# Performance work log

Hardware: AMD Instinct MI355X
Metric: run time of the kernel (lower is better)

## Reference

```python
import jax, jax.numpy as jnp
import numpy as np

N = 131072          # total atoms/nodes
LSQ = 9             # (lmax+1)^2 spherical coefficients
C = 128             # sphere_channels
H = 1024            # hidden_channels
NUM_MOLS = 2048     # number of molecules (len(natoms))


def setup_inputs() -> dict:
    key = jax.random.key(0)
    ks = jax.random.split(key, 8)
    node_embedding = jax.random.normal(ks[0], (N, LSQ, C), dtype=jnp.float32)
    batch = jnp.sort(jax.random.randint(ks[1], (N,), 0, NUM_MOLS, dtype=jnp.int64))
    natoms = jax.random.randint(ks[2], (NUM_MOLS,), 1, 100, dtype=jnp.int64)
    # MLP parameters (Linear weights stored as [in, out] for x @ W + b)
    s1 = 1.0 / np.sqrt(C)
    s2 = 1.0 / np.sqrt(H)
    W1 = jax.random.uniform(ks[3], (C, H), jnp.float32, -s1, s1)
    b1 = jnp.zeros((H,), jnp.float32)
    W2 = jax.random.uniform(ks[4], (H, H), jnp.float32, -s2, s2)
    b2 = jnp.zeros((H,), jnp.float32)
    W3 = jax.random.uniform(ks[5], (H, 1), jnp.float32, -s2, s2)
    b3 = jnp.zeros((1,), jnp.float32)
    return {"node_embedding": node_embedding, "W1": W1, "b1": b1,
            "W2": W2, "b2": b2, "W3": W3, "b3": b3,
            "batch": batch, "natoms": natoms}


def reference(node_embedding, W1, b1, W2, b2, W3, b3, batch, natoms):
    # take l=0 coefficient: [N, C]
    x = node_embedding[:, 0, :]
    h = jax.nn.silu(x @ W1 + b1)          # [N, H]
    h = jax.nn.silu(h @ W2 + b2)          # [N, H]
    node_energy = (h @ W3 + b3)[:, 0]     # [N]
    # scatter-sum per molecule (index_add_)
    energy = jax.ops.segment_sum(node_energy, batch, num_segments=NUM_MOLS)
    return energy  # reduce == 'sum'
```

## Files before the change

### kernel.cpp

```cpp
#include <hip/hip_runtime.h>

typedef unsigned short u16;
typedef __attribute__((ext_vector_type(8))) short bf16x8;
typedef __attribute__((ext_vector_type(4))) float f32x4;

#define NROWS 131072
#define NMOL  2048
#define CIN   128
#define HDIM  1024
#define BM    64
#define EMBSTRIDE 1152

__device__ __forceinline__ u16 f2bf(float f) {
    union { float f; unsigned u; } v; v.f = f;
    unsigned u = v.u;
    u += 0x7FFFu + ((u >> 16) & 1u);
    return (u16)(u >> 16);
}

__device__ __forceinline__ float silu_f(float v) {
    float e = __expf(-v);
    return v * __builtin_amdgcn_rcpf(1.0f + e);
}

__device__ __forceinline__ f32x4 mfma16(bf16x8 a, bf16x8 b, f32x4 c) {
    return __builtin_amdgcn_mfma_f32_16x16x32_bf16(a, b, c, 0, 0, 0);
}

__global__ void pack_w(const float* __restrict__ W, u16* __restrict__ dst, int K, int N) {
    int tid  = blockIdx.x * blockDim.x + threadIdx.x;
    int lane = tid & 63;
    int frag = tid >> 6;
    int KT = K >> 5;
    int NT = N >> 4;
    if (frag >= KT * NT) return;
    int kt = frag % KT;
    int nt = frag / KT;
    int col  = (nt << 4) + (lane & 15);
    int krow = (kt << 5) + ((lane >> 4) << 3);
    __align__(16) u16 tmp[8];
    #pragma unroll
    for (int j = 0; j < 8; ++j) tmp[j] = f2bf(W[(size_t)(krow + j) * N + col]);
    *reinterpret_cast<uint4*>(dst + (size_t)tid * 8) = *reinterpret_cast<uint4*>(tmp);
}

__global__ __launch_bounds__(512, 2) void fused_mlp(
    const float* __restrict__ emb,
    const u16*  __restrict__ w1f,
    const u16*  __restrict__ w2f,
    const float* __restrict__ b1,
    const float* __restrict__ b2,
    const float* __restrict__ w3,
    const float* __restrict__ b3,
    float* __restrict__ node_e)
{
    __shared__ u16  x_lds[BM][CIN + 8];
    __shared__ u16  h1_lds[BM][HDIM + 8];
    __shared__ float e_red[8][BM];

    const int tid  = threadIdx.x;
    const int lane = tid & 63;
    const int w    = tid >> 6;
    const int row0 = blockIdx.x * BM;

    {
        int r   = tid >> 3;
        int seg = tid & 7;
        const float4* s4 = reinterpret_cast<const float4*>(
            emb + (size_t)(row0 + r) * EMBSTRIDE + seg * 16);
        __align__(16) u16 u[16];
        #pragma unroll
        for (int i = 0; i < 4; ++i) {
            float4 f = s4[i];
            u[i*4+0] = f2bf(f.x); u[i*4+1] = f2bf(f.y);
            u[i*4+2] = f2bf(f.z); u[i*4+3] = f2bf(f.w);
        }
        uint4* d = reinterpret_cast<uint4*>(&x_lds[r][seg * 16]);
        d[0] = reinterpret_cast<uint4*>(u)[0];
        d[1] = reinterpret_cast<uint4*>(u)[1];
        reinterpret_cast<float*>(e_red)[tid] = 0.0f;
    }
    __syncthreads();

    {
        bf16x8 a1[4][4];
        #pragma unroll
        for (int mt = 0; mt < 4; ++mt)
            #pragma unroll
            for (int kt = 0; kt < 4; ++kt)
                a1[mt][kt] = *reinterpret_cast<const bf16x8*>(
                    &x_lds[mt*16 + (lane & 15)][kt*32 + ((lane >> 4) << 3)]);

        #pragma unroll
        for (int ntl = 0; ntl < 8; ++ntl) {
            int nt  = w * 8 + ntl;
            int col = nt * 16 + (lane & 15);
            float bias = b1[col];
            f32x4 acc[4];
            #pragma unroll
            for (int mt = 0; mt < 4; ++mt) acc[mt] = (f32x4){0.f, 0.f, 0.f, 0.f};
            #pragma unroll
            for (int kt = 0; kt < 4; ++kt) {
                bf16x8 bfrag = *reinterpret_cast<const bf16x8*>(
                    w1f + ((size_t)(nt * 4 + kt) * 64 + lane) * 8);
                #pragma unroll
                for (int mt = 0; mt < 4; ++mt)
                    acc[mt] = mfma16(a1[mt][kt], bfrag, acc[mt]);
            }
            #pragma unroll
            for (int mt = 0; mt < 4; ++mt)
                #pragma unroll
                for (int j = 0; j < 4; ++j) {
                    float s = silu_f(acc[mt][j] + bias);
                    h1_lds[mt*16 + (lane >> 4)*4 + j][col] = f2bf(s);
                }
        }
    }
    __syncthreads();

    float e_lane[16];
    #pragma unroll
    for (int i = 0; i < 16; ++i) e_lane[i] = 0.0f;

    const u16* aptr = &h1_lds[lane & 15][(lane >> 4) << 3];

    #pragma unroll
    for (int c = 0; c < 2; ++c) {
        int ntbase = w * 8 + c * 4;
        f32x4 acc[4][4];
        #pragma unroll
        for (int mt = 0; mt < 4; ++mt)
            #pragma unroll
            for (int nti = 0; nti < 4; ++nti) acc[mt][nti] = (f32x4){0.f, 0.f, 0.f, 0.f};

        #pragma unroll 2
        for (int kt = 0; kt < 32; ++kt) {
            bf16x8 a[4];
            #pragma unroll
            for (int mt = 0; mt < 4; ++mt)
                a[mt] = *reinterpret_cast<const bf16x8*>(aptr + mt*16*(HDIM+8) + kt*32);
            #pragma unroll
            for (int nti = 0; nti < 4; ++nti) {
                bf16x8 b = *reinterpret_cast<const bf16x8*>(
                    w2f + (((size_t)(ntbase + nti) * 32 + kt) * 64 + lane) * 8);
                #pragma unroll
                for (int mt = 0; mt < 4; ++mt)
                    acc[mt][nti] = mfma16(a[mt], b, acc[mt][nti]);
            }
        }
        #pragma unroll
        for (int nti = 0; nti < 4; ++nti) {
            int col = (ntbase + nti) * 16 + (lane & 15);
            float bias = b2[col];
            float w3v  = w3[col];
            #pragma unroll
            for (int mt = 0; mt < 4; ++mt)
                #pragma unroll
                for (int j = 0; j < 4; ++j) {
                    float s = silu_f(acc[mt][nti][j] + bias);
                    e_lane[mt*4 + j] += s * w3v;
                }
        }
    }

    #pragma unroll
    for (int off = 1; off < 16; off <<= 1)
        #pragma unroll
        for (int i = 0; i < 16; ++i)
            e_lane[i] += __shfl_xor(e_lane[i], off, 64);

    if ((lane & 15) == 0) {
        int g = lane >> 4;
        #pragma unroll
        for (int mt = 0; mt < 4; ++mt)
            #pragma unroll
            for (int j = 0; j < 4; ++j)
                e_red[w][mt*16 + g*4 + j] = e_lane[mt*4 + j];
    }
    __syncthreads();

    if (tid < BM) {
        float s = 0.0f;
        #pragma unroll
        for (int ww = 0; ww < 8; ++ww) s += e_red[ww][tid];
        node_e[row0 + tid] = s + b3[0];
    }
}

__global__ void segsum(const float* __restrict__ node_e,
                       const int* __restrict__ batch,
                       float* __restrict__ out)
{
    int mol  = blockIdx.x;
    int lane = threadIdx.x;

    int lo = 0, hi = NROWS;
    while (lo < hi) { int mid = (lo + hi) >> 1; if (batch[mid] < mol)     lo = mid + 1; else hi = mid; }
    int start = lo;
    lo = start; hi = NROWS;
    while (lo < hi) { int mid = (lo + hi) >> 1; if (batch[mid] < mol + 1) lo = mid + 1; else hi = mid; }
    int end = lo;

    float s = 0.0f;
    for (int i = start + lane; i < end; i += 64) s += node_e[i];
    #pragma unroll
    for (int off = 32; off; off >>= 1) s += __shfl_xor(s, off, 64);
    if (lane == 0) out[mol] = s;
}

extern "C" void kernel_launch(void* const* d_in, const int* in_sizes, int n_in,
                              void* d_out, int out_size, void* d_ws, size_t ws_size,
                              hipStream_t stream) {
    const float* emb = (const float*)d_in[0];
    const float* W1  = (const float*)d_in[1];
    const float* b1  = (const float*)d_in[2];
    const float* W2  = (const float*)d_in[3];
    const float* b2  = (const float*)d_in[4];
    const float* W3  = (const float*)d_in[5];
    const float* b3  = (const float*)d_in[6];
    const int*   batch = (const int*)d_in[7];

    u16* w1f = (u16*)d_ws;
    u16* w2f = (u16*)((char*)d_ws + (size_t)CIN * HDIM * 2);
    float* node_e = (float*)((char*)d_ws + (size_t)CIN * HDIM * 2 + (size_t)HDIM * HDIM * 2);

    pack_w<<<64,  256, 0, stream>>>(W1, w1f, CIN,  HDIM);
    pack_w<<<512, 256, 0, stream>>>(W2, w2f, HDIM, HDIM);
    fused_mlp<<<NROWS / BM, 512, 0, stream>>>(emb, w1f, w2f, b1, b2, W3, b3, node_e);
    segsum<<<NMOL, 64, 0, stream>>>(node_e, batch, (float*)d_out);
}
```

Before: 337.6 us.

## Switch fused MLP to 32x32x16 MFMA tiles with software-pipelined operand loads

Replaces the 16x16x32 bf16 MFMA tiling with 32x32x16 tiles, so each wave covers 64 rows by 128 columns in a single pass. The weight packing layout is rewritten to match. Weight and activation fragments are double-buffered, loading step k+1 or k+2 while step k computes, to hide global and LDS load latency. The larger accumulators raise register pressure, and the wider 32-lane shuffle reduction adds work in the epilogue.

```diff
diff --git a/kernel.cpp b/kernel.cpp
--- a/kernel.cpp
+++ b/kernel.cpp
@@ -1,8 +1,8 @@
 #include <hip/hip_runtime.h>
 
 typedef unsigned short u16;
-typedef __attribute__((ext_vector_type(8))) short bf16x8;
-typedef __attribute__((ext_vector_type(4))) float f32x4;
+typedef __attribute__((ext_vector_type(8)))  short bf16x8;
+typedef __attribute__((ext_vector_type(16))) float f32x16;
 
 #define NROWS 131072
 #define NMOL  2048
@@ -11,6 +11,10 @@
 #define BM    64
 #define EMBSTRIDE 1152
 
+#define KT1 (CIN  / 16)
+#define KT2 (HDIM / 16)
+#define NT  (HDIM / 32)
+
 __device__ __forceinline__ u16 f2bf(float f) {
     union { float f; unsigned u; } v; v.f = f;
     unsigned u = v.u;
@@ -23,21 +27,21 @@
     return v * __builtin_amdgcn_rcpf(1.0f + e);
 }
 
-__device__ __forceinline__ f32x4 mfma16(bf16x8 a, bf16x8 b, f32x4 c) {
-    return __builtin_amdgcn_mfma_f32_16x16x32_bf16(a, b, c, 0, 0, 0);
-}
-
-__global__ void pack_w(const float* __restrict__ W, u16* __restrict__ dst, int K, int N) {
+__device__ __forceinline__ f32x16 mfma32(bf16x8 a, bf16x8 b, f32x16 c) {
+    return __builtin_amdgcn_mfma_f32_32x32x16_bf16(a, b, c, 0, 0, 0);
+}
+
+__global__ void pack_w32(const float* __restrict__ W, u16* __restrict__ dst, int K, int N) {
     int tid  = blockIdx.x * blockDim.x + threadIdx.x;
     int lane = tid & 63;
     int frag = tid >> 6;
-    int KT = K >> 5;
-    int NT = N >> 4;
-    if (frag >= KT * NT) return;
-    int kt = frag % KT;
-    int nt = frag / KT;
-    int col  = (nt << 4) + (lane & 15);
-    int krow = (kt << 5) + ((lane >> 4) << 3);
+    int NTl = N >> 5;
+    int KTl = K >> 4;
+    if (frag >= KTl * NTl) return;
+    int kt = frag / NTl;
+    int nt = frag - kt * NTl;
+    int col  = (nt << 5) + (lane & 31);
+    int krow = (kt << 4) + ((lane >> 5) << 3);
     __align__(16) u16 tmp[8];
     #pragma unroll
     for (int j = 0; j < 8; ++j) tmp[j] = f2bf(W[(size_t)(krow + j) * N + col]);
@@ -61,6 +65,8 @@
     const int tid  = threadIdx.x;
     const int lane = tid & 63;
     const int w    = tid >> 6;
+    const int l31  = lane & 31;
+    const int lhi  = lane >> 5;
     const int row0 = blockIdx.x * BM;
 
     {
@@ -78,104 +84,156 @@
         uint4* d = reinterpret_cast<uint4*>(&x_lds[r][seg * 16]);
         d[0] = reinterpret_cast<uint4*>(u)[0];
         d[1] = reinterpret_cast<uint4*>(u)[1];
-        reinterpret_cast<float*>(e_red)[tid] = 0.0f;
-    }
+    }
+
+    auto LDB1 = [&](int kt, bf16x8* b) {
+        #pragma unroll
+        for (int nti = 0; nti < 4; ++nti)
+            b[nti] = *reinterpret_cast<const bf16x8*>(
+                w1f + (((size_t)kt * NT + w * 4 + nti) * 64 + lane) * 8);
+    };
+    auto LDB2 = [&](int kt, bf16x8* b) {
+        #pragma unroll
+        for (int nti = 0; nti < 4; ++nti)
+            b[nti] = *reinterpret_cast<const bf16x8*>(
+                w2f + (((size_t)kt * NT + w * 4 + nti) * 64 + lane) * 8);
+    };
+
+    bf16x8 bC[4], bN[4];
+    LDB1(0, bC);
     __syncthreads();
 
     {
-        bf16x8 a1[4][4];
-        #pragma unroll
-        for (int mt = 0; mt < 4; ++mt)
-            #pragma unroll
-            for (int kt = 0; kt < 4; ++kt)
-                a1[mt][kt] = *reinterpret_cast<const bf16x8*>(
-                    &x_lds[mt*16 + (lane & 15)][kt*32 + ((lane >> 4) << 3)]);
-
-        #pragma unroll
-        for (int ntl = 0; ntl < 8; ++ntl) {
-            int nt  = w * 8 + ntl;
-            int col = nt * 16 + (lane & 15);
+        f32x16 acc1[2][4];
+        #pragma unroll
+        for (int mt = 0; mt < 2; ++mt)
+            #pragma unroll
+            for (int nti = 0; nti < 4; ++nti)
+                #pragma unroll
+                for (int r = 0; r < 16; ++r) acc1[mt][nti][r] = 0.0f;
+
+        #pragma unroll
+        for (int kt = 0; kt < KT1; ++kt) {
+            if (kt + 1 < KT1) LDB1(kt + 1, bN);
+            bf16x8 a[2];
+            #pragma unroll
+            for (int mt = 0; mt < 2; ++mt)
+                a[mt] = *reinterpret_cast<const bf16x8*>(
+                    &x_lds[mt*32 + l31][kt*16 + (lhi << 3)]);
+            #pragma unroll
+            for (int nti = 0; nti < 4; ++nti)
+                #pragma unroll
+                for (int mt = 0; mt < 2; ++mt)
+                    acc1[mt][nti] = mfma32(a[mt], bC[nti], acc1[mt][nti]);
+            if (kt + 1 < KT1) {
+                #pragma unroll
+                for (int i = 0; i < 4; ++i) bC[i] = bN[i];
+            }
+        }
+
+        #pragma unroll
+        for (int nti = 0; nti < 4; ++nti) {
+            int col = w*128 + nti*32 + l31;
             float bias = b1[col];
-            f32x4 acc[4];
-            #pragma unroll
-            for (int mt = 0; mt < 4; ++mt) acc[mt] = (f32x4){0.f, 0.f, 0.f, 0.f};
-            #pragma unroll
-            for (int kt = 0; kt < 4; ++kt) {
-                bf16x8 bfrag = *reinterpret_cast<const bf16x8*>(
-                    w1f + ((size_t)(nt * 4 + kt) * 64 + lane) * 8);
-                #pragma unroll
-                for (int mt = 0; mt < 4; ++mt)
-                    acc[mt] = mfma16(a1[mt][kt], bfrag, acc[mt]);
-            }
-            #pragma unroll
-            for (int mt = 0; mt < 4; ++mt)
-                #pragma unroll
-                for (int j = 0; j < 4; ++j) {
-                    float s = silu_f(acc[mt][j] + bias);
-                    h1_lds[mt*16 + (lane >> 4)*4 + j][col] = f2bf(s);
+            #pragma unroll
+            for (int mt = 0; mt < 2; ++mt)
+                #pragma unroll
+                for (int r = 0; r < 16; ++r) {
+                    int row = mt*32 + (r & 3) + 8*(r >> 2) + 4*lhi;
+                    h1_lds[row][col] = f2bf(silu_f(acc1[mt][nti][r] + bias));
                 }
         }
     }
+
+    LDB2(0, bC);
+    LDB2(1, bN);
     __syncthreads();
 
-    float e_lane[16];
-    #pragma unroll
-    for (int i = 0; i < 16; ++i) e_lane[i] = 0.0f;
-
-    const u16* aptr = &h1_lds[lane & 15][(lane >> 4) << 3];
-
-    #pragma unroll
-    for (int c = 0; c < 2; ++c) {
-        int ntbase = w * 8 + c * 4;
-        f32x4 acc[4][4];
-        #pragma unroll
-        for (int mt = 0; mt < 4; ++mt)
-            #pragma unroll
-            for (int nti = 0; nti < 4; ++nti) acc[mt][nti] = (f32x4){0.f, 0.f, 0.f, 0.f};
-
-        #pragma unroll 2
-        for (int kt = 0; kt < 32; ++kt) {
-            bf16x8 a[4];
-            #pragma unroll
-            for (int mt = 0; mt < 4; ++mt)
-                a[mt] = *reinterpret_cast<const bf16x8*>(aptr + mt*16*(HDIM+8) + kt*32);
-            #pragma unroll
-            for (int nti = 0; nti < 4; ++nti) {
-                bf16x8 b = *reinterpret_cast<const bf16x8*>(
-                    w2f + (((size_t)(ntbase + nti) * 32 + kt) * 64 + lane) * 8);
-                #pragma unroll
-                for (int mt = 0; mt < 4; ++mt)
-                    acc[mt][nti] = mfma16(a[mt], b, acc[mt][nti]);
+    auto LDA2 = [&](int kt, bf16x8* a) {
+        #pragma unroll
+        for (int mt = 0; mt < 2; ++mt)
+            a[mt] = *reinterpret_cast<const bf16x8*>(
+                &h1_lds[mt*32 + l31][kt*16 + (lhi << 3)]);
+    };
+
+    f32x16 acc[2][4];
+    #pragma unroll
+    for (int mt = 0; mt < 2; ++mt)
+        #pragma unroll
+        for (int nti = 0; nti < 4; ++nti)
+            #pragma unroll
+            for (int r = 0; r < 16; ++r) acc[mt][nti][r] = 0.0f;
+
+    bf16x8 aC[2], aN[2];
+    LDA2(0, aC);
+    LDA2(1, aN);
+
+    #pragma unroll 4
+    for (int kt = 0; kt < KT2 - 2; kt += 2) {
+        bf16x8 aP[2], bP[4];
+        LDB2(kt + 2, bP);
+        LDA2(kt + 2, aP);
+        #pragma unroll
+        for (int nti = 0; nti < 4; ++nti)
+            #pragma unroll
+            for (int mt = 0; mt < 2; ++mt)
+                acc[mt][nti] = mfma32(aC[mt], bC[nti], acc[mt][nti]);
+        bf16x8 aQ[2], bQ[4];
+        LDB2(kt + 3, bQ);
+        LDA2(kt + 3, aQ);
+        #pragma unroll
+        for (int nti = 0; nti < 4; ++nti)
+            #pragma unroll
+            for (int mt = 0; mt < 2; ++mt)
+                acc[mt][nti] = mfma32(aN[mt], bN[nti], acc[mt][nti]);
+        #pragma unroll
+        for (int i = 0; i < 2; ++i) { aC[i] = aP[i]; aN[i] = aQ[i]; }
+        #pragma unroll
+        for (int i = 0; i < 4; ++i) { bC[i] = bP[i]; bN[i] = bQ[i]; }
+    }
+    #pragma unroll
+    for (int nti = 0; nti < 4; ++nti)
+        #pragma unroll
+        for (int mt = 0; mt < 2; ++mt)
+            acc[mt][nti] = mfma32(aC[mt], bC[nti], acc[mt][nti]);
+    #pragma unroll
+    for (int nti = 0; nti < 4; ++nti)
+        #pragma unroll
+        for (int mt = 0; mt < 2; ++mt)
+            acc[mt][nti] = mfma32(aN[mt], bN[nti], acc[mt][nti]);
+
+    float e_lane[32];
+    #pragma unroll
+    for (int i = 0; i < 32; ++i) e_lane[i] = 0.0f;
+
+    #pragma unroll
+    for (int nti = 0; nti < 4; ++nti) {
+        int col = w*128 + nti*32 + l31;
+        float bias = b2[col];
+        float w3v  = w3[col];
+        #pragma unroll
+        for (int mt = 0; mt < 2; ++mt)
+            #pragma unroll
+            for (int r = 0; r < 16; ++r) {
+                float s = silu_f(acc[mt][nti][r] + bias);
+                e_lane[mt*16 + r] += s * w3v;
             }
-        }
-        #pragma unroll
-        for (int nti = 0; nti < 4; ++nti) {
-            int col = (ntbase + nti) * 16 + (lane & 15);
-            float bias = b2[col];
-            float w3v  = w3[col];
-            #pragma unroll
-            for (int mt = 0; mt < 4; ++mt)
-                #pragma unroll
-                for (int j = 0; j < 4; ++j) {
-                    float s = silu_f(acc[mt][nti][j] + bias);
-                    e_lane[mt*4 + j] += s * w3v;
-                }
-        }
-    }
-
-    #pragma unroll
-    for (int off = 1; off < 16; off <<= 1)
-        #pragma unroll
-        for (int i = 0; i < 16; ++i)
+    }
+
+    #pragma unroll
+    for (int off = 1; off < 32; off <<= 1)
+        #pragma unroll
+        for (int i = 0; i < 32; ++i)
             e_lane[i] += __shfl_xor(e_lane[i], off, 64);
 
-    if ((lane & 15) == 0) {
-        int g = lane >> 4;
-        #pragma unroll
-        for (int mt = 0; mt < 4; ++mt)
-            #pragma unroll
-            for (int j = 0; j < 4; ++j)
-                e_red[w][mt*16 + g*4 + j] = e_lane[mt*4 + j];
+    if (l31 == 0) {
+        #pragma unroll
+        for (int mt = 0; mt < 2; ++mt)
+            #pragma unroll
+            for (int r = 0; r < 16; ++r) {
+                int row = mt*32 + (r & 3) + 8*(r >> 2) + 4*lhi;
+                e_red[w][row] = e_lane[mt*16 + r];
+            }
     }
     __syncthreads();
 
@@ -224,8 +282,8 @@
     u16* w2f = (u16*)((char*)d_ws + (size_t)CIN * HDIM * 2);
     float* node_e = (float*)((char*)d_ws + (size_t)CIN * HDIM * 2 + (size_t)HDIM * HDIM * 2);
 
-    pack_w<<<64,  256, 0, stream>>>(W1, w1f, CIN,  HDIM);
-    pack_w<<<512, 256, 0, stream>>>(W2, w2f, HDIM, HDIM);
+    pack_w32<<<64,  256, 0, stream>>>(W1, w1f, CIN,  HDIM);
+    pack_w32<<<512, 256, 0, stream>>>(W2, w2f, HDIM, HDIM);
     fused_mlp<<<NROWS / BM, 512, 0, stream>>>(emb, w1f, w2f, b1, b2, W3, b3, node_e);
     segsum<<<NMOL, 64, 0, stream>>>(node_e, batch, (float*)d_out);
 }
```

Measured after the change: 364.9 us. 1.08x slower.
